# Kernel tuning notes

Measured on AMD Instinct MI355X. Metric: run time of the kernel, lower is better.

The kernel has to match this reference:

```python
import jax, jax.numpy as jnp
import numpy as np

HIDDEN = 2048
INTER = 4096
NUM_EXPERTS = 8
TOP_K = 4
BATCH, SEQ = 2, 2048
TOKENS = BATCH * SEQ


def setup_inputs() -> dict:
    key = jax.random.key(0)
    k_x, k_rw, k_tw, k_te, k_gu, k_dn = jax.random.split(key, 6)
    x = jax.random.normal(k_x, (BATCH, SEQ, HIDDEN), dtype=jnp.float32)
    # full router weights (passed through but unused by this patched forward)
    weights = jax.random.uniform(k_rw, (TOKENS, NUM_EXPERTS), dtype=jnp.float32)
    tw = jax.random.uniform(k_tw, (TOKENS, TOP_K), dtype=jnp.float32)
    top_weights = tw / jnp.sum(tw, axis=-1, keepdims=True)  # softmax-like, renormalize=False downstream
    top_experts = jax.random.randint(k_te, (TOKENS, TOP_K), 0, NUM_EXPERTS, dtype=jnp.int64)
    scale_gu = 1.0 / np.sqrt(HIDDEN)
    scale_dn = 1.0 / np.sqrt(INTER)
    gate_up_weights = jax.random.normal(k_gu, (NUM_EXPERTS, 2 * INTER, HIDDEN), dtype=jnp.float32) * scale_gu
    down_weights = jax.random.normal(k_dn, (NUM_EXPERTS, HIDDEN, INTER), dtype=jnp.float32) * scale_dn
    return {
        'x': x,
        'weights': weights,
        'top_weights': top_weights,
        'top_experts': top_experts,
        'gate_up_weights': gate_up_weights,
        'down_weights': down_weights,
    }


def _fused_moe(xf, gate_up_weights, down_weights, top_weights, top_experts):
    """xf: [T, D]. Dense per-expert loop (scan over experts), masked combine.

    Matches fused_moe(renormalize=False): out[t] = sum_k top_weights[t,k] * expert_{top_experts[t,k]}(x[t])
    expert(x) = (silu(x @ Wg^T) * (x @ Wu^T)) @ Wd^T with [Wg; Wu] = gate_up.
    """
    E = gate_up_weights.shape[0]

    def step(out, inp):
        w_gu, w_d, e = inp
        # per-token combine coefficient for this expert (0 if not routed)
        coef = jnp.sum(jnp.where(top_experts == e, top_weights, 0.0), axis=-1)  # [T]
        h = xf @ w_gu.T                       # [T, 2*INTER]
        gate, up = jnp.split(h, 2, axis=-1)
        act = jax.nn.silu(gate) * up          # [T, INTER]
        o = act @ w_d.T                       # [T, D]
        return out + coef[:, None] * o, None

    out, _ = jax.lax.scan(step, jnp.zeros_like(xf),
                          (gate_up_weights, down_weights, jnp.arange(E, dtype=jnp.int64)))
    return out


def reference(x, weights, top_weights, top_experts, gate_up_weights, down_weights):
    B, S, D = x.shape
    xf = x.reshape(-1, D)  # flatten(0, 1)
    out = _fused_moe(xf, gate_up_weights, down_weights, top_weights, top_experts)
    return out.reshape(B, S, D)  # unflatten(0, (-1, q_len))
```

## Files before the change

### kernel.cpp

```cpp
#include <hip/hip_runtime.h>
#include <stdint.h>

#define T_TOKENS 4096
#define D_HID    2048
#define D_INT    4096
#define N_EXP    8
#define TOPK     4
#define NFLAT    (T_TOKENS*TOPK)
#define BMT      256
#define MAXPAD   (NFLAT + N_EXP*BMT)
#define MT2      (MAXPAD/BMT)

#define OFF_PTOK 0ull
#define OFF_PWT  73728ull
#define OFF_CNT  147456ull
#define OFF_TOFF 147712ull
#define OFF_SEG  155904ull
#define OFF_XB   262144ull
#define OFF_ACT  17039360ull
#define OFF_W    168034304ull

typedef float f32x4  __attribute__((ext_vector_type(4)));
typedef short bf16x8 __attribute__((ext_vector_type(8)));

__device__ __forceinline__ unsigned short f2bf(float f) {
    unsigned int u = __float_as_uint(f);
    u += 0x7fffu + ((u >> 16) & 1u);
    return (unsigned short)(u >> 16);
}

__device__ __forceinline__ void gload_lds16(const void* g, void* l) {
    __builtin_amdgcn_global_load_lds((const __attribute__((address_space(1))) void*)g,
                                     (__attribute__((address_space(3))) void*)l,
                                     16, 0, 0);
}

__device__ __forceinline__ int xcd_logical(int hw, int nwg) {
    int q = nwg >> 3, r = nwg & 7;
    int xc = hw & 7, sl = hw >> 3;
    return (xc < r ? xc * (q + 1) : r * (q + 1) + (xc - r) * q) + sl;
}

__global__ void k_prep(const float* __restrict__ x, unsigned short* __restrict__ xb,
                       float* __restrict__ out) {
    int i = blockIdx.x * 256 + threadIdx.x;
    float4 v = ((const float4*)x)[i];
    ushort4 h;
    h.x = f2bf(v.x); h.y = f2bf(v.y); h.z = f2bf(v.z); h.w = f2bf(v.w);
    ((ushort4*)xb)[i] = h;
    ((float4*)out)[i] = make_float4(0.f, 0.f, 0.f, 0.f);
}

__global__ void k_cast(const float* __restrict__ src, unsigned short* __restrict__ dst) {
    size_t i = (size_t)blockIdx.x * 256 + threadIdx.x;
    float4 v = ((const float4*)src)[i];
    ushort4 h;
    h.x = f2bf(v.x); h.y = f2bf(v.y); h.z = f2bf(v.z); h.w = f2bf(v.w);
    ((ushort4*)dst)[i] = h;
}

__global__ void k_count(const int* __restrict__ te, int* __restrict__ counts,
                        int* __restrict__ toff) {
    int e = blockIdx.x, t = threadIdx.x;
    int cnt = 0;
    int base = t * 64;
    for (int i = 0; i < 64; i++) cnt += (te[base + i] == e);
    __shared__ int s[256];
    s[t] = cnt; __syncthreads();
    int incl = cnt;
    for (int off = 1; off < 256; off <<= 1) {
        int tmp = (t >= off) ? s[t - off] : 0;
        __syncthreads();
        incl += tmp; s[t] = incl;
        __syncthreads();
    }
    toff[e * 256 + t] = incl - cnt;
    if (t == 255) counts[e] = incl;
}

__global__ void k_fill(const int* __restrict__ te, const float* __restrict__ tw,
                       const int* __restrict__ counts, const int* __restrict__ toff,
                       int* __restrict__ ptok, float* __restrict__ pwt, int* __restrict__ seg) {
    int e = blockIdx.x, t = threadIdx.x;
    int segs[9]; int a = 0;
    #pragma unroll
    for (int j = 0; j < 8; j++) { segs[j] = a; a += (counts[j] + BMT - 1) & ~(BMT - 1); }
    segs[8] = a;
    if (e == 0 && t == 0) { for (int j = 0; j < 9; j++) seg[j] = segs[j]; }
    int base = segs[e] + toff[e * 256 + t];
    int rank = 0;
    for (int i = t * 64; i < (t + 1) * 64; i++) {
        if (te[i] == e) { ptok[base + rank] = i >> 2; pwt[base + rank] = tw[i]; rank++; }
    }
    int cnt = counts[e], pc = (cnt + BMT - 1) & ~(BMT - 1);
    for (int i = cnt + t; i < pc; i += 256) { ptok[segs[e] + i] = -1; pwt[segs[e] + i] = 0.f; }
}


#define MFMA_2M(M0, M1) \
    _Pragma("unroll") for (int n_ = 0; n_ < 4; ++n_) \
        acc[M0][n_] = __builtin_amdgcn_mfma_f32_16x16x32_bf16(af[M0], bf[n_], acc[M0][n_], 0, 0, 0); \
    _Pragma("unroll") for (int n_ = 0; n_ < 4; ++n_) \
        acc[M1][n_] = __builtin_amdgcn_mfma_f32_16x16x32_bf16(af[M1], bf[n_], acc[M1][n_], 0, 0, 0);

#define KSTEP(VMS) \
  asm volatile("s_waitcnt vmcnt(" VMS ")" ::: "memory"); \
  __builtin_amdgcn_s_barrier(); \
  __builtin_amdgcn_sched_barrier(0); \
  { \
    const char* pT = ldsc + (cb << 15); \
    bf16x8 af[8], bf[4]; \
    _Pragma("unroll") for (int n_ = 0; n_ < 4; ++n_) \
        bf[n_] = *(const bf16x8*)(pT + b_off + n_ * 1024); \
    af[0] = *(const bf16x8*)(pT + a_off); \
    af[1] = *(const bf16x8*)(pT + a_off + 1024); \
    __builtin_amdgcn_sched_barrier(0); \
    _Pragma("unroll") for (int m_ = 2; m_ < 8; ++m_) \
        af[m_] = *(const bf16x8*)(pT + a_off + m_ * 1024); \
    __builtin_amdgcn_sched_barrier(0); \
    asm volatile("s_waitcnt lgkmcnt(6)" ::: "memory"); \
    __builtin_amdgcn_sched_barrier(0); \
    __builtin_amdgcn_s_setprio(1); \
    MFMA_2M(0, 1) \
    __builtin_amdgcn_s_setprio(0); \
    asm volatile("s_waitcnt lgkmcnt(4)" ::: "memory"); \
    __builtin_amdgcn_sched_barrier(0); \
    __builtin_amdgcn_s_setprio(1); \
    MFMA_2M(2, 3) \
    __builtin_amdgcn_s_setprio(0); \
    asm volatile("s_waitcnt lgkmcnt(2)" ::: "memory"); \
    __builtin_amdgcn_sched_barrier(0); \
    __builtin_amdgcn_s_setprio(1); \
    MFMA_2M(4, 5) \
    __builtin_amdgcn_s_setprio(0); \
    asm volatile("s_waitcnt lgkmcnt(0)" ::: "memory"); \
    __builtin_amdgcn_sched_barrier(0); \
    __builtin_amdgcn_s_barrier(); \
    __builtin_amdgcn_s_setprio(1); \
    MFMA_2M(6, 7) \
    __builtin_amdgcn_s_setprio(0); \
    cb = (cb + 1) & 3; \
  }

__global__ void __launch_bounds__(512, 2)
k_g1(const unsigned short* __restrict__ xb, const unsigned short* __restrict__ wgu_b,
     const int* __restrict__ ptok, const int* __restrict__ seg,
     unsigned short* __restrict__ act) {
    extern __shared__ char smem[];
    char* ldsw = smem; const char* ldsc = smem;
    int logical = xcd_logical(blockIdx.x, 2304);
    int nb = logical / MT2, mb = logical % MT2;
    if (mb * BMT >= seg[8]) return;
    int e = 0;
    #pragma unroll
    for (int j = 1; j < 8; ++j) if (seg[j] <= mb * BMT) e = j;
    int tid = threadIdx.x, w = tid >> 6, l = tid & 63;
    int wr = w >> 2, wc = w & 3;

    int g = (l & 3) ^ ((l >> 3) & 3);
    int r0 = w * 16 + (l >> 2), r1 = 128 + r0;
    int t0 = ptok[mb * BMT + r0]; if (t0 < 0) t0 = 0;
    int t1 = ptok[mb * BMT + r1]; if (t1 < 0) t1 = 0;
    const char* pa0 = (const char*)xb + (size_t)t0 * 4096 + g * 16;
    const char* pa1 = (const char*)xb + (size_t)t1 * 4096 + g * 16;
    int wcr0 = r0 >> 6, j0 = r0 & 63;
    int wcr1 = r1 >> 6, j1 = r1 & 63;
    int gr0 = (j0 < 32) ? (nb * 128 + wcr0 * 32 + j0) : (D_INT + nb * 128 + wcr0 * 32 + j0 - 32);
    int gr1 = (j1 < 32) ? (nb * 128 + wcr1 * 32 + j1) : (D_INT + nb * 128 + wcr1 * 32 + j1 - 32);
    const char* wbase = (const char*)wgu_b + (size_t)e * 8192 * 4096;
    const char* pb0 = wbase + (size_t)gr0 * 4096 + g * 16;
    const char* pb1 = wbase + (size_t)gr1 * 4096 + g * 16;
    int dA0 = w * 1024, dA1 = 8192 + w * 1024;
    int dB0 = 16384 + w * 1024, dB1 = 24576 + w * 1024;
    int sb = 0;
    auto STAGE = [&]() {
        char* d = ldsw + (sb << 15);
        gload_lds16(pa0, d + dA0); gload_lds16(pa1, d + dA1);
        gload_lds16(pb0, d + dB0); gload_lds16(pb1, d + dB1);
        pa0 += 64; pa1 += 64; pb0 += 64; pb1 += 64;
        sb = (sb + 1) & 3;
    };

    int off_frag = (l & 15) * 64 + ((((l >> 4)) ^ (((l & 15) >> 1) & 3)) << 4);
    int a_off = wr * 8192 + off_frag;
    int b_off = 16384 + wc * 4096 + off_frag;

    f32x4 acc[8][4];
    #pragma unroll
    for (int m = 0; m < 8; ++m)
        #pragma unroll
        for (int n = 0; n < 4; ++n) acc[m][n] = (f32x4){0.f, 0.f, 0.f, 0.f};

    int cb = 0;
    STAGE(); STAGE(); STAGE();
    for (int kt = 0; kt < 61; ++kt) { STAGE(); KSTEP("12") }
    KSTEP("8") KSTEP("4") KSTEP("0")

    int mbase = mb * BMT;
    #pragma unroll
    for (int m = 0; m < 8; ++m) {
        int rowl = wr * 128 + m * 16 + (l >> 4) * 4;
        #pragma unroll
        for (int np = 0; np < 2; ++np) {
            int col = nb * 128 + wc * 32 + np * 16 + (l & 15);
            #pragma unroll
            for (int r = 0; r < 4; ++r) {
                float gv = acc[m][np][r], uv = acc[m][np + 2][r];
                float av = gv / (1.f + __expf(-gv)) * uv;
                act[(size_t)(mbase + rowl + r) * D_INT + col] = f2bf(av);
            }
        }
    }
}

__global__ void __launch_bounds__(512, 2)
k_g2(const unsigned short* __restrict__ act, const unsigned short* __restrict__ wd_b,
     const int* __restrict__ ptok, const float* __restrict__ pwt,
     const int* __restrict__ seg, float* __restrict__ out) {
    extern __shared__ char smem[];
    char* ldsw = smem; const char* ldsc = smem;
    int logical = xcd_logical(blockIdx.x, 1152);
    int pair = logical / MT2, mb = logical % MT2;
    int nb = pair >> 1, ks = pair & 1;
    if (mb * BMT >= seg[8]) return;
    int e = 0;
    #pragma unroll
    for (int j = 1; j < 8; ++j) if (seg[j] <= mb * BMT) e = j;
    int tid = threadIdx.x, w = tid >> 6, l = tid & 63;
    int wr = w >> 2, wc = w & 3;
    int koff = ks * 4096;

    int g = (l & 3) ^ ((l >> 3) & 3);
    int r0 = w * 16 + (l >> 2), r1 = 128 + r0;
    const char* pa0 = (const char*)act + (size_t)(mb * BMT + r0) * 8192 + koff + g * 16;
    const char* pa1 = (const char*)act + (size_t)(mb * BMT + r1) * 8192 + koff + g * 16;
    const char* wbase = (const char*)wd_b + (size_t)e * D_HID * 8192;
    const char* pb0 = wbase + (size_t)(nb * 256 + r0) * 8192 + koff + g * 16;
    const char* pb1 = wbase + (size_t)(nb * 256 + r1) * 8192 + koff + g * 16;
    int dA0 = w * 1024, dA1 = 8192 + w * 1024;
    int dB0 = 16384 + w * 1024, dB1 = 24576 + w * 1024;
    int sb = 0;
    auto STAGE = [&]() {
        char* d = ldsw + (sb << 15);
        gload_lds16(pa0, d + dA0); gload_lds16(pa1, d + dA1);
        gload_lds16(pb0, d + dB0); gload_lds16(pb1, d + dB1);
        pa0 += 64; pa1 += 64; pb0 += 64; pb1 += 64;
        sb = (sb + 1) & 3;
    };

    int off_frag = (l & 15) * 64 + ((((l >> 4)) ^ (((l & 15) >> 1) & 3)) << 4);
    int a_off = wr * 8192 + off_frag;
    int b_off = 16384 + wc * 4096 + off_frag;

    f32x4 acc[8][4];
    #pragma unroll
    for (int m = 0; m < 8; ++m)
        #pragma unroll
        for (int n = 0; n < 4; ++n) acc[m][n] = (f32x4){0.f, 0.f, 0.f, 0.f};

    int cb = 0;
    STAGE(); STAGE(); STAGE();
    for (int kt = 0; kt < 61; ++kt) { STAGE(); KSTEP("12") }
    KSTEP("8") KSTEP("4") KSTEP("0")

    #pragma unroll
    for (int m = 0; m < 8; ++m) {
        int rowl = wr * 128 + m * 16 + (l >> 4) * 4;
        #pragma unroll
        for (int r = 0; r < 4; ++r) {
            int p = mb * BMT + rowl + r;
            int tok = ptok[p];
            float wt = pwt[p];
            if (tok >= 0) {
                #pragma unroll
                for (int n = 0; n < 4; ++n) {
                    int col = nb * 256 + wc * 64 + n * 16 + (l & 15);
                    unsafeAtomicAdd(&out[(size_t)tok * D_HID + col], wt * acc[m][n][r]);
                }
            }
        }
    }
}

extern "C" void kernel_launch(void* const* d_in, const int* in_sizes, int n_in,
                              void* d_out, int out_size, void* d_ws, size_t ws_size,
                              hipStream_t stream) {
    const float* x   = (const float*)d_in[0];
    const float* tw  = (const float*)d_in[2];
    const int*   te  = (const int*)d_in[3];
    const float* wgu = (const float*)d_in[4];
    const float* wd  = (const float*)d_in[5];
    float* out = (float*)d_out;
    char*  ws  = (char*)d_ws;

    int*   ptok   = (int*)(ws + OFF_PTOK);
    float* pwt    = (float*)(ws + OFF_PWT);
    int*   counts = (int*)(ws + OFF_CNT);
    int*   toff   = (int*)(ws + OFF_TOFF);
    int*   seg    = (int*)(ws + OFF_SEG);
    unsigned short* xb  = (unsigned short*)(ws + OFF_XB);
    unsigned short* act = (unsigned short*)(ws + OFF_ACT);
    unsigned short* w_b = (unsigned short*)(ws + OFF_W);

    hipFuncSetAttribute((const void*)k_g1, hipFuncAttributeMaxDynamicSharedMemorySize, 131072);
    hipFuncSetAttribute((const void*)k_g2, hipFuncAttributeMaxDynamicSharedMemorySize, 131072);

    k_prep<<<8192, 256, 0, stream>>>(x, xb, out);
    k_count<<<N_EXP, 256, 0, stream>>>(te, counts, toff);
    k_fill<<<N_EXP, 256, 0, stream>>>(te, tw, counts, toff, ptok, pwt, seg);

    k_cast<<<131072, 256, 0, stream>>>(wgu, w_b);
    k_g1<<<2304, 512, 131072, stream>>>(xb, w_b, ptok, seg, act);
    k_cast<<<65536, 256, 0, stream>>>(wd, w_b);
    k_g2<<<1152, 512, 131072, stream>>>(act, w_b, ptok, pwt, seg, out);
}
```

Before: 1.282 ms.

## Shrink GEMM tiles to 256x128 with 4 waves and triple-buffered LDS

Both grouped GEMM kernels move from 512-thread blocks with 256x256 tiles and a 4-stage 32KB LDS ring to 256-thread blocks with 256x128 tiles and a 3-stage 24KB ring. Grid sizes double to match, and the prologue and epilogue waitcnt counts are adjusted for the shallower pipeline. The aim is lower LDS use per block so more blocks fit per CU, plus finer work granularity across CUs. The cost is less operand reuse per tile, so more global and LDS traffic per FLOP, and one fewer prefetch stage to hide latency.

```diff
diff --git a/kernel.cpp b/kernel.cpp
--- a/kernel.cpp
+++ b/kernel.cpp
@@ -108,7 +108,7 @@
   __builtin_amdgcn_s_barrier(); \
   __builtin_amdgcn_sched_barrier(0); \
   { \
-    const char* pT = ldsc + (cb << 15); \
+    const char* pT = ldsc + cb * 24576; \
     bf16x8 af[8], bf[4]; \
     _Pragma("unroll") for (int n_ = 0; n_ < 4; ++n_) \
         bf[n_] = *(const bf16x8*)(pT + b_off + n_ * 1024); \
@@ -139,46 +139,53 @@
     __builtin_amdgcn_s_setprio(1); \
     MFMA_2M(6, 7) \
     __builtin_amdgcn_s_setprio(0); \
-    cb = (cb + 1) & 3; \
+    cb = (cb == 2) ? 0 : cb + 1; \
   }
 
-__global__ void __launch_bounds__(512, 2)
+__global__ void __launch_bounds__(256, 2)
 k_g1(const unsigned short* __restrict__ xb, const unsigned short* __restrict__ wgu_b,
      const int* __restrict__ ptok, const int* __restrict__ seg,
      unsigned short* __restrict__ act) {
     extern __shared__ char smem[];
     char* ldsw = smem; const char* ldsc = smem;
-    int logical = xcd_logical(blockIdx.x, 2304);
+    int logical = xcd_logical(blockIdx.x, 4608);
     int nb = logical / MT2, mb = logical % MT2;
     if (mb * BMT >= seg[8]) return;
     int e = 0;
     #pragma unroll
     for (int j = 1; j < 8; ++j) if (seg[j] <= mb * BMT) e = j;
     int tid = threadIdx.x, w = tid >> 6, l = tid & 63;
-    int wr = w >> 2, wc = w & 3;
+    int wr = w >> 1, wc = w & 1;
 
     int g = (l & 3) ^ ((l >> 3) & 3);
-    int r0 = w * 16 + (l >> 2), r1 = 128 + r0;
-    int t0 = ptok[mb * BMT + r0]; if (t0 < 0) t0 = 0;
-    int t1 = ptok[mb * BMT + r1]; if (t1 < 0) t1 = 0;
-    const char* pa0 = (const char*)xb + (size_t)t0 * 4096 + g * 16;
-    const char* pa1 = (const char*)xb + (size_t)t1 * 4096 + g * 16;
-    int wcr0 = r0 >> 6, j0 = r0 & 63;
-    int wcr1 = r1 >> 6, j1 = r1 & 63;
-    int gr0 = (j0 < 32) ? (nb * 128 + wcr0 * 32 + j0) : (D_INT + nb * 128 + wcr0 * 32 + j0 - 32);
-    int gr1 = (j1 < 32) ? (nb * 128 + wcr1 * 32 + j1) : (D_INT + nb * 128 + wcr1 * 32 + j1 - 32);
+    const char* pa[4]; const char* pb[2];
+    #pragma unroll
+    for (int i = 0; i < 4; ++i) {
+        int r = i * 64 + w * 16 + (l >> 2);
+        int tok = ptok[mb * BMT + r]; if (tok < 0) tok = 0;
+        pa[i] = (const char*)xb + (size_t)tok * 4096 + g * 16;
+    }
     const char* wbase = (const char*)wgu_b + (size_t)e * 8192 * 4096;
-    const char* pb0 = wbase + (size_t)gr0 * 4096 + g * 16;
-    const char* pb1 = wbase + (size_t)gr1 * 4096 + g * 16;
-    int dA0 = w * 1024, dA1 = 8192 + w * 1024;
-    int dB0 = 16384 + w * 1024, dB1 = 24576 + w * 1024;
+    #pragma unroll
+    for (int j = 0; j < 2; ++j) {
+        int r = j * 64 + w * 16 + (l >> 2);
+        int wcr = r >> 6, jj = r & 63;
+        int grow = (jj < 32) ? (nb * 64 + wcr * 32 + jj)
+                             : (D_INT + nb * 64 + wcr * 32 + jj - 32);
+        pb[j] = wbase + (size_t)grow * 4096 + g * 16;
+    }
     int sb = 0;
     auto STAGE = [&]() {
-        char* d = ldsw + (sb << 15);
-        gload_lds16(pa0, d + dA0); gload_lds16(pa1, d + dA1);
-        gload_lds16(pb0, d + dB0); gload_lds16(pb1, d + dB1);
-        pa0 += 64; pa1 += 64; pb0 += 64; pb1 += 64;
-        sb = (sb + 1) & 3;
+        char* d = ldsw + sb * 24576;
+        gload_lds16(pa[0], d + w * 1024);
+        gload_lds16(pa[1], d + 4096 + w * 1024);
+        gload_lds16(pa[2], d + 8192 + w * 1024);
+        gload_lds16(pa[3], d + 12288 + w * 1024);
+        gload_lds16(pb[0], d + 16384 + w * 1024);
+        gload_lds16(pb[1], d + 20480 + w * 1024);
+        pa[0] += 64; pa[1] += 64; pa[2] += 64; pa[3] += 64;
+        pb[0] += 64; pb[1] += 64;
+        sb = (sb == 2) ? 0 : sb + 1;
     };
 
     int off_frag = (l & 15) * 64 + ((((l >> 4)) ^ (((l & 15) >> 1) & 3)) << 4);
@@ -192,9 +199,9 @@
         for (int n = 0; n < 4; ++n) acc[m][n] = (f32x4){0.f, 0.f, 0.f, 0.f};
 
     int cb = 0;
-    STAGE(); STAGE(); STAGE();
-    for (int kt = 0; kt < 61; ++kt) { STAGE(); KSTEP("12") }
-    KSTEP("8") KSTEP("4") KSTEP("0")
+    STAGE(); STAGE();
+    for (int kt = 0; kt < 62; ++kt) { STAGE(); KSTEP("12") }
+    KSTEP("6") KSTEP("0")
 
     int mbase = mb * BMT;
     #pragma unroll
@@ -202,7 +209,7 @@
         int rowl = wr * 128 + m * 16 + (l >> 4) * 4;
         #pragma unroll
         for (int np = 0; np < 2; ++np) {
-            int col = nb * 128 + wc * 32 + np * 16 + (l & 15);
+            int col = nb * 64 + wc * 32 + np * 16 + (l & 15);
             #pragma unroll
             for (int r = 0; r < 4; ++r) {
                 float gv = acc[m][np][r], uv = acc[m][np + 2][r];
@@ -213,13 +220,13 @@
     }
 }
 
-__global__ void __launch_bounds__(512, 2)
+__global__ void __launch_bounds__(256, 2)
 k_g2(const unsigned short* __restrict__ act, const unsigned short* __restrict__ wd_b,
      const int* __restrict__ ptok, const float* __restrict__ pwt,
      const int* __restrict__ seg, float* __restrict__ out) {
     extern __shared__ char smem[];
     char* ldsw = smem; const char* ldsc = smem;
-    int logical = xcd_logical(blockIdx.x, 1152);
+    int logical = xcd_logical(blockIdx.x, 2304);
     int pair = logical / MT2, mb = logical % MT2;
     int nb = pair >> 1, ks = pair & 1;
     if (mb * BMT >= seg[8]) return;
@@ -227,25 +234,34 @@
     #pragma unroll
     for (int j = 1; j < 8; ++j) if (seg[j] <= mb * BMT) e = j;
     int tid = threadIdx.x, w = tid >> 6, l = tid & 63;
-    int wr = w >> 2, wc = w & 3;
+    int wr = w >> 1, wc = w & 1;
     int koff = ks * 4096;
 
     int g = (l & 3) ^ ((l >> 3) & 3);
-    int r0 = w * 16 + (l >> 2), r1 = 128 + r0;
-    const char* pa0 = (const char*)act + (size_t)(mb * BMT + r0) * 8192 + koff + g * 16;
-    const char* pa1 = (const char*)act + (size_t)(mb * BMT + r1) * 8192 + koff + g * 16;
+    const char* pa[4]; const char* pb[2];
+    #pragma unroll
+    for (int i = 0; i < 4; ++i) {
+        int r = i * 64 + w * 16 + (l >> 2);
+        pa[i] = (const char*)act + (size_t)(mb * BMT + r) * 8192 + koff + g * 16;
+    }
     const char* wbase = (const char*)wd_b + (size_t)e * D_HID * 8192;
-    const char* pb0 = wbase + (size_t)(nb * 256 + r0) * 8192 + koff + g * 16;
-    const char* pb1 = wbase + (size_t)(nb * 256 + r1) * 8192 + koff + g * 16;
-    int dA0 = w * 1024, dA1 = 8192 + w * 1024;
-    int dB0 = 16384 + w * 1024, dB1 = 24576 + w * 1024;
+    #pragma unroll
+    for (int j = 0; j < 2; ++j) {
+        int r = j * 64 + w * 16 + (l >> 2);
+        pb[j] = wbase + (size_t)(nb * 128 + r) * 8192 + koff + g * 16;
+    }
     int sb = 0;
     auto STAGE = [&]() {
-        char* d = ldsw + (sb << 15);
-        gload_lds16(pa0, d + dA0); gload_lds16(pa1, d + dA1);
-        gload_lds16(pb0, d + dB0); gload_lds16(pb1, d + dB1);
-        pa0 += 64; pa1 += 64; pb0 += 64; pb1 += 64;
-        sb = (sb + 1) & 3;
+        char* d = ldsw + sb * 24576;
+        gload_lds16(pa[0], d + w * 1024);
+        gload_lds16(pa[1], d + 4096 + w * 1024);
+        gload_lds16(pa[2], d + 8192 + w * 1024);
+        gload_lds16(pa[3], d + 12288 + w * 1024);
+        gload_lds16(pb[0], d + 16384 + w * 1024);
+        gload_lds16(pb[1], d + 20480 + w * 1024);
+        pa[0] += 64; pa[1] += 64; pa[2] += 64; pa[3] += 64;
+        pb[0] += 64; pb[1] += 64;
+        sb = (sb == 2) ? 0 : sb + 1;
     };
 
     int off_frag = (l & 15) * 64 + ((((l >> 4)) ^ (((l & 15) >> 1) & 3)) << 4);
@@ -259,9 +275,9 @@
         for (int n = 0; n < 4; ++n) acc[m][n] = (f32x4){0.f, 0.f, 0.f, 0.f};
 
     int cb = 0;
-    STAGE(); STAGE(); STAGE();
-    for (int kt = 0; kt < 61; ++kt) { STAGE(); KSTEP("12") }
-    KSTEP("8") KSTEP("4") KSTEP("0")
+    STAGE(); STAGE();
+    for (int kt = 0; kt < 62; ++kt) { STAGE(); KSTEP("12") }
+    KSTEP("6") KSTEP("0")
 
     #pragma unroll
     for (int m = 0; m < 8; ++m) {
@@ -274,7 +290,7 @@
             if (tok >= 0) {
                 #pragma unroll
                 for (int n = 0; n < 4; ++n) {
-                    int col = nb * 256 + wc * 64 + n * 16 + (l & 15);
+                    int col = nb * 128 + wc * 64 + n * 16 + (l & 15);
                     unsafeAtomicAdd(&out[(size_t)tok * D_HID + col], wt * acc[m][n][r]);
                 }
             }
@@ -302,15 +318,15 @@
     unsigned short* act = (unsigned short*)(ws + OFF_ACT);
     unsigned short* w_b = (unsigned short*)(ws + OFF_W);
 
-    hipFuncSetAttribute((const void*)k_g1, hipFuncAttributeMaxDynamicSharedMemorySize, 131072);
-    hipFuncSetAttribute((const void*)k_g2, hipFuncAttributeMaxDynamicSharedMemorySize, 131072);
+    hipFuncSetAttribute((const void*)k_g1, hipFuncAttributeMaxDynamicSharedMemorySize, 73728);
+    hipFuncSetAttribute((const void*)k_g2, hipFuncAttributeMaxDynamicSharedMemorySize, 73728);
 
     k_prep<<<8192, 256, 0, stream>>>(x, xb, out);
     k_count<<<N_EXP, 256, 0, stream>>>(te, counts, toff);
     k_fill<<<N_EXP, 256, 0, stream>>>(te, tw, counts, toff, ptok, pwt, seg);
 
     k_cast<<<131072, 256, 0, stream>>>(wgu, w_b);
-    k_g1<<<2304, 512, 131072, stream>>>(xb, w_b, ptok, seg, act);
+    k_g1<<<4608, 256, 73728, stream>>>(xb, w_b, ptok, seg, act);
     k_cast<<<65536, 256, 0, stream>>>(wd, w_b);
-    k_g2<<<1152, 512, 131072, stream>>>(act, w_b, ptok, pwt, seg, out);
-}
+    k_g2<<<2304, 256, 73728, stream>>>(act, w_b, ptok, pwt, seg, out);
+}
```

After: 1.264 ms. Within noise of the previous version (-1.4%).
